# Kernel tuning notes

Hardware: AMD Instinct MI355X
Metric: run time of the kernel (lower is better)

The kernel has to match this reference:

```python
import jax, jax.numpy as jnp
import numpy as np

H = 1024  # hidden_size
B, N = 64, 512
NEG = 1e30


def setup_inputs() -> dict:
    key = jax.random.key(0)
    ks = jax.random.split(key, 10)
    Q = jax.random.normal(ks[0], (B, H), dtype=jnp.float32)
    K = jax.random.normal(ks[1], (B, N, H), dtype=jnp.float32)
    V = jax.random.normal(ks[2], (B, N, H), dtype=jnp.float32)
    adj = jax.random.randint(ks[3], (B, N), 0, 2, dtype=jnp.int32)
    s_mask = jax.random.randint(ks[4], (B, N), 0, 2, dtype=jnp.int32)
    o_mask = jax.random.randint(ks[5], (B, N), 0, 2, dtype=jnp.int32)
    # learned params (torch nn.Linear conventions: y = x @ W.T + b)
    lim = 1.0 / np.sqrt(2 * H)
    W_att = jax.random.uniform(ks[6], (1, 2 * H), minval=-lim, maxval=lim, dtype=jnp.float32)
    b_att = jax.random.uniform(ks[7], (1,), minval=-lim, maxval=lim, dtype=jnp.float32)
    limh = 1.0 / np.sqrt(H)
    Wr0 = jax.random.uniform(ks[8], (H, H), minval=-limh, maxval=limh, dtype=jnp.float32)
    Wr1 = jax.random.uniform(ks[9], (H, H), minval=-limh, maxval=limh, dtype=jnp.float32)
    return {"Q": Q, "K": K, "V": V, "adj": adj, "s_mask": s_mask, "o_mask": o_mask,
            "W_att": W_att, "b_att": b_att, "Wr0": Wr0, "Wr1": Wr1}


def reference(Q, K, V, adj, s_mask, o_mask, W_att, b_att, Wr0, Wr1):
    # concat-score: Linear([Q;K]) == Q @ Wq.T + K @ Wk.T + b (avoids materializing [B,N,2H])
    Wq, Wk = W_att[:, :H], W_att[:, H:]  # each [1, H]
    q_score = Q @ Wq.T                    # [B, 1]
    k_score = jnp.einsum('bnh,oh->bn', K, Wk)  # [B, N]
    alpha = (q_score + k_score + b_att)[:, None, :]  # [B, 1, N]
    # adjacency mask
    adj_f = adj.astype(jnp.float32)[:, None, :]      # [B, 1, N]
    alpha = alpha - (1.0 - adj_f) * NEG
    attn_weight = jax.nn.softmax(alpha, axis=2)      # [B, 1, N]
    # dual value projections gated by speaker/other masks
    V0 = jnp.einsum('bnh,oh->bno', V, Wr0)           # [B, N, H]
    V1 = jnp.einsum('bnh,oh->bno', V, Wr1)
    s = s_mask.astype(jnp.float32)[:, :, None]
    o = o_mask.astype(jnp.float32)[:, :, None]
    Vg = V0 * s + V1 * o                             # [B, N, H]
    attn_sum = jnp.einsum('bon,bnh->boh', attn_weight, Vg)[:, 0]  # [B, H]
    return (attn_weight, attn_sum)
```

## Files before the change

### kernel.cpp

```cpp
#include <hip/hip_runtime.h>
#include <math.h>

#define HDIM 1024
#define INVB (1 << 13)
#define SBIT (1 << 14)
#define OBIT (1 << 15)
#define SLOTS 10
#define CH 32

__global__ __launch_bounds__(256) void k_fusedA(const float* __restrict__ Kmat,
                                                const float* __restrict__ V,
                                                const int* __restrict__ adj,
                                                const int* __restrict__ sm,
                                                const int* __restrict__ om,
                                                const float* __restrict__ Wk,
                                                float* __restrict__ e_out,
                                                float* __restrict__ p0,
                                                float* __restrict__ p1) {
    __shared__ int segc[8];
    __shared__ int codeL[CH];
    __shared__ float2 eso[CH];
    __shared__ float2 cw[CH + 8];
    __shared__ int cn[CH + 8];
    __shared__ int s_cnz8;
    int b = blockIdx.x / SLOTS;
    int chunk = blockIdx.x - b * SLOTS;
    int tid = threadIdx.x, wave = tid >> 6, lane = tid & 63;
    int gb = b * 512;
    int start = chunk * CH;
    size_t pbase = ((size_t)(chunk * 64 + b)) * HDIM + tid * 4;

    int r0w = wave * 128;
    int a0p = adj[gb + r0w + lane] != 0;
    int a1p = adj[gb + r0w + 64 + lane] != 0;
    unsigned long long m0 = __ballot(a0p);
    unsigned long long m1 = __ballot(a1p);
    if (lane == 0) {
        segc[wave * 2]     = __popcll(m0);
        segc[wave * 2 + 1] = __popcll(m1);
    }
    __syncthreads();
    int tot = 0;
#pragma unroll
    for (int i = 0; i < 8; ++i) tot += segc[i];
    int kp = (tot + CH - 1) & ~(CH - 1);
    if (start >= kp) {
        float4 z = {0.f, 0.f, 0.f, 0.f};
        *(float4*)(p0 + pbase) = z;
        *(float4*)(p1 + pbase) = z;
        return;
    }
    {
        unsigned long long lt = (1ull << lane) - 1ull;
        int base = 0;
#pragma unroll
        for (int i = 0; i < 8; ++i) if (i < wave * 2) base += segc[i];
        int pos0 = base + __popcll(m0 & lt);
        if (a0p && pos0 >= start && pos0 < start + CH) {
            int r = r0w + lane;
            codeL[pos0 - start] = r | (sm[gb + r] ? SBIT : 0) | (om[gb + r] ? OBIT : 0);
        }
        int base1 = base + __popcll(m0);
        int pos1 = base1 + __popcll(m1 & lt);
        if (a1p && pos1 >= start && pos1 < start + CH) {
            int r = r0w + 64 + lane;
            codeL[pos1 - start] = r | (sm[gb + r] ? SBIT : 0) | (om[gb + r] ? OBIT : 0);
        }
    }
    if (tid < CH && start + tid >= tot) codeL[tid] = INVB;
    const float4* wk4 = (const float4*)Wk;
    float4 wk0 = wk4[lane], wk1 = wk4[64 + lane],
           wk2 = wk4[128 + lane], wk3 = wk4[192 + lane];
    __syncthreads();

#pragma unroll
    for (int pp = 0; pp < 4; ++pp) {
        int rr = wave * 8 + pp * 2;
        int c0 = codeL[rr], c1 = codeL[rr + 1];
        int n0 = c0 & 511, n1 = c1 & 511;
        const float4* kq0 = (const float4*)(Kmat + (size_t)(gb + n0) * HDIM);
        const float4* kq1 = (const float4*)(Kmat + (size_t)(gb + n1) * HDIM);
        float4 a0 = kq0[lane],       a1 = kq0[64 + lane],
               a2 = kq0[128 + lane], a3 = kq0[192 + lane];
        float4 d0 = kq1[lane],       d1 = kq1[64 + lane],
               d2 = kq1[128 + lane], d3 = kq1[192 + lane];
        __builtin_amdgcn_sched_barrier(0);

        float s0 = 0.f, s1 = 0.f;
        s0 = fmaf(a0.x, wk0.x, s0); s0 = fmaf(a0.y, wk0.y, s0);
        s0 = fmaf(a0.z, wk0.z, s0); s0 = fmaf(a0.w, wk0.w, s0);
        s0 = fmaf(a1.x, wk1.x, s0); s0 = fmaf(a1.y, wk1.y, s0);
        s0 = fmaf(a1.z, wk1.z, s0); s0 = fmaf(a1.w, wk1.w, s0);
        s0 = fmaf(a2.x, wk2.x, s0); s0 = fmaf(a2.y, wk2.y, s0);
        s0 = fmaf(a2.z, wk2.z, s0); s0 = fmaf(a2.w, wk2.w, s0);
        s0 = fmaf(a3.x, wk3.x, s0); s0 = fmaf(a3.y, wk3.y, s0);
        s0 = fmaf(a3.z, wk3.z, s0); s0 = fmaf(a3.w, wk3.w, s0);
        s1 = fmaf(d0.x, wk0.x, s1); s1 = fmaf(d0.y, wk0.y, s1);
        s1 = fmaf(d0.z, wk0.z, s1); s1 = fmaf(d0.w, wk0.w, s1);
        s1 = fmaf(d1.x, wk1.x, s1); s1 = fmaf(d1.y, wk1.y, s1);
        s1 = fmaf(d1.z, wk1.z, s1); s1 = fmaf(d1.w, wk1.w, s1);
        s1 = fmaf(d2.x, wk2.x, s1); s1 = fmaf(d2.y, wk2.y, s1);
        s1 = fmaf(d2.z, wk2.z, s1); s1 = fmaf(d2.w, wk2.w, s1);
        s1 = fmaf(d3.x, wk3.x, s1); s1 = fmaf(d3.y, wk3.y, s1);
        s1 = fmaf(d3.z, wk3.z, s1); s1 = fmaf(d3.w, wk3.w, s1);

#pragma unroll
        for (int off = 32; off; off >>= 1) {
            s0 += __shfl_xor(s0, off);
            s1 += __shfl_xor(s1, off);
        }
        if (lane == 0) {
            float e0 = expf(s0), e1 = expf(s1);
            if (!(c0 & INVB)) e_out[gb + n0] = e0;
            if (!(c1 & INVB)) e_out[gb + n1] = e1;
            eso[rr]     = make_float2((c0 & SBIT) ? e0 : 0.f, (c0 & OBIT) ? e0 : 0.f);
            eso[rr + 1] = make_float2((c1 & SBIT) ? e1 : 0.f, (c1 & OBIT) ? e1 : 0.f);
        }
    }
    __syncthreads();

    if (wave == 0) {
        bool pred = (lane < CH) && ((codeL[lane] & (SBIT | OBIT)) != 0) &&
                    !(codeL[lane] & INVB);
        unsigned long long m = __ballot(pred);
        int cnz = __popcll(m);
        if (pred) {
            int pos = __popcll(m & ((1ull << lane) - 1ull));
            cn[pos] = codeL[lane] & 511;
            cw[pos] = eso[lane];
        }
        int cnz8 = (cnz + 7) & ~7;
        if (lane >= CH && lane < CH + 8) {
            int p = cnz + (lane - CH);
            if (p < cnz8) { cn[p] = 0; cw[p] = make_float2(0.f, 0.f); }
        }
        if (lane == 0) s_cnz8 = cnz8;
    }
    __syncthreads();

    int cnz8 = s_cnz8;
    const float* Vb = V + (size_t)gb * HDIM;
    float4 a0 = {0.f, 0.f, 0.f, 0.f};
    float4 a1 = {0.f, 0.f, 0.f, 0.f};
    for (int g = 0; g < cnz8; g += 8) {
        int nn[8]; float2 ww[8];
#pragma unroll
        for (int i = 0; i < 8; ++i) { nn[i] = cn[g + i]; ww[i] = cw[g + i]; }
        float4 v[8];
#pragma unroll
        for (int i = 0; i < 8; ++i)
            v[i] = *((const float4*)(Vb + (size_t)nn[i] * HDIM) + tid);
        __builtin_amdgcn_sched_barrier(0);
#pragma unroll
        for (int i = 0; i < 8; ++i) {
            a0.x = fmaf(ww[i].x, v[i].x, a0.x); a0.y = fmaf(ww[i].x, v[i].y, a0.y);
            a0.z = fmaf(ww[i].x, v[i].z, a0.z); a0.w = fmaf(ww[i].x, v[i].w, a0.w);
            a1.x = fmaf(ww[i].y, v[i].x, a1.x); a1.y = fmaf(ww[i].y, v[i].y, a1.y);
            a1.z = fmaf(ww[i].y, v[i].z, a1.z); a1.w = fmaf(ww[i].y, v[i].w, a1.w);
        }
    }
    *(float4*)(p0 + pbase) = a0;
    *(float4*)(p1 + pbase) = a1;
}

__global__ __launch_bounds__(512) void k_denomredu(const float* __restrict__ e,
                                                   const int* __restrict__ adj,
                                                   const float* __restrict__ p0,
                                                   const float* __restrict__ p1,
                                                   float* __restrict__ w_out,
                                                   float* __restrict__ u0,
                                                   float* __restrict__ u1) {
    __shared__ float red[8];
    int b = blockIdx.x;
    int tid = threadIdx.x;
    int wave = tid >> 6, lane = tid & 63;
    int idx = b * 512 + tid;

    float ev = adj[idx] ? e[idx] : 0.f;
    float t = ev;
#pragma unroll
    for (int off = 32; off; off >>= 1) t += __shfl_xor(t, off);
    if (lane == 0) red[wave] = t;
    __syncthreads();
    float tot = red[0];
#pragma unroll
    for (int i = 1; i < 8; ++i) tot += red[i];
    float inv = 1.f / tot;
    w_out[idx] = ev * inv;

    const float* p = (tid < 256) ? p0 : p1;
    float* u = (tid < 256) ? u0 : u1;
    int h4 = tid & 255;
    float4 a = {0.f, 0.f, 0.f, 0.f};
#pragma unroll
    for (int s = 0; s < SLOTS; ++s) {
        float4 v = *(const float4*)(p + ((size_t)(s * 64 + b)) * HDIM + h4 * 4);
        a.x += v.x; a.y += v.y; a.z += v.z; a.w += v.w;
    }
    a.x *= inv; a.y *= inv; a.z *= inv; a.w *= inv;
    *(float4*)(u + (size_t)b * HDIM + h4 * 4) = a;
}

__global__ __launch_bounds__(256) void k_out(const float* __restrict__ u0,
                                             const float* __restrict__ u1,
                                             const float* __restrict__ Wr0,
                                             const float* __restrict__ Wr1,
                                             float* __restrict__ pOut) {
    __shared__ float lds[64 * 128];
    int tid = threadIdx.x;
    int ht = blockIdx.x >> 4;
    int kc = blockIdx.x & 15;
    const float* usrc = (kc < 8) ? u0 : u1;
    const float* wsrc = (kc < 8) ? Wr0 : Wr1;
    int koff = (kc & 7) * 128;
    int h0 = ht * 64;

    {
        int c4 = tid & 31;
        int r2 = tid >> 5;
#pragma unroll
        for (int i = 0; i < 8; ++i) {
            int row = i * 8 + r2;
            float4 v = *(const float4*)(usrc + (size_t)row * HDIM + koff + c4 * 4);
            *(float4*)&lds[row * 128 + ((c4 ^ (row & 7)) << 2)] = v;
        }
    }
    __syncthreads();

    int b = tid & 63;
    int wu = __builtin_amdgcn_readfirstlane(tid >> 6);
    int hbase = h0 + wu * 16;
    const float* wrow = wsrc + (size_t)hbase * HDIM + koff;

    float acc[16];
#pragma unroll
    for (int j = 0; j < 16; ++j) acc[j] = 0.f;

#pragma unroll 4
    for (int k4 = 0; k4 < 32; ++k4) {
        float4 uv = *(float4*)&lds[b * 128 + ((k4 ^ (b & 7)) << 2)];
#pragma unroll
        for (int j = 0; j < 16; ++j) {
            float4 wv = *(const float4*)(wrow + (size_t)j * HDIM + k4 * 4);
            acc[j] = fmaf(uv.x, wv.x, acc[j]);
            acc[j] = fmaf(uv.y, wv.y, acc[j]);
            acc[j] = fmaf(uv.z, wv.z, acc[j]);
            acc[j] = fmaf(uv.w, wv.w, acc[j]);
        }
    }
#pragma unroll
    for (int j = 0; j < 16; ++j)
        pOut[((size_t)kc * HDIM + hbase + j) * 64 + b] = acc[j];
}

__global__ __launch_bounds__(256) void k_redout(const float* __restrict__ pOut,
                                                float* __restrict__ out1) {
    int tid = threadIdx.x;
    int b = tid & 63;
    int h = blockIdx.x * 4 + (tid >> 6);
    float acc = 0.f;
#pragma unroll
    for (int kc = 0; kc < 16; ++kc)
        acc += pOut[((size_t)kc * HDIM + h) * 64 + b];
    out1[(size_t)b * HDIM + h] = acc;
}

extern "C" void kernel_launch(void* const* d_in, const int* in_sizes, int n_in,
                              void* d_out, int out_size, void* d_ws, size_t ws_size,
                              hipStream_t stream) {
    const float* Kmat  = (const float*)d_in[1];
    const float* V     = (const float*)d_in[2];
    const int*   adj   = (const int*)d_in[3];
    const int*   smask = (const int*)d_in[4];
    const int*   omask = (const int*)d_in[5];
    const float* Watt  = (const float*)d_in[6];
    const float* Wr0   = (const float*)d_in[8];
    const float* Wr1   = (const float*)d_in[9];
    float* out = (float*)d_out;
    float* ws  = (float*)d_ws;

    float* e    = ws;
    float* p0   = ws + 32768;
    float* p1   = ws + 688128;
    float* u0   = ws + 1343488;
    float* u1   = ws + 1409024;
    float* pOut = ws + 1474560;
    const float* Wk = Watt + HDIM;

    k_fusedA   <<<64 * SLOTS, 256, 0, stream>>>(Kmat, V, adj, smask, omask, Wk, e, p0, p1);
    k_denomredu<<<        64, 512, 0, stream>>>(e, adj, p0, p1, out, u0, u1);
    k_out      <<<       256, 256, 0, stream>>>(u0, u1, Wr0, Wr1, pOut);
    k_redout   <<<       256, 256, 0, stream>>>(pOut, out + 32768);
}
```

Before: 63.45 us.

## Split score and weighted-V passes; partition V gather by hidden octant

The fused score+V-gather kernel is split into three kernels: one computes exp scores for adjacent rows, one computes the softmax denominator and weights, and a new weighted-V kernel compacts the active rows per batch. Each block of that kernel handles one 128-column slice of H and reduces partial sums in LDS. This removes the large per-chunk partial buffers (p0/p1) and their cross-slot reduction pass, and V blocks no longer depend on the chunk split of the score pass. In exchange it adds a kernel launch and rereads e, adj and the masks from global memory.

Measured after the change: 64.13 us. No clear change (+1.1%).

```diff
diff --git a/kernel.cpp b/kernel.cpp
--- a/kernel.cpp
+++ b/kernel.cpp
@@ -3,32 +3,20 @@
 
 #define HDIM 1024
 #define INVB (1 << 13)
-#define SBIT (1 << 14)
-#define OBIT (1 << 15)
-#define SLOTS 10
-#define CH 32
-
-__global__ __launch_bounds__(256) void k_fusedA(const float* __restrict__ Kmat,
-                                                const float* __restrict__ V,
-                                                const int* __restrict__ adj,
-                                                const int* __restrict__ sm,
-                                                const int* __restrict__ om,
-                                                const float* __restrict__ Wk,
-                                                float* __restrict__ e_out,
-                                                float* __restrict__ p0,
-                                                float* __restrict__ p1) {
+#define SCH 32
+#define SSLOTS 10
+
+__global__ __launch_bounds__(256) void k_scoresE(const float* __restrict__ Kmat,
+                                                 const int* __restrict__ adj,
+                                                 const float* __restrict__ Wk,
+                                                 float* __restrict__ e_out) {
     __shared__ int segc[8];
-    __shared__ int codeL[CH];
-    __shared__ float2 eso[CH];
-    __shared__ float2 cw[CH + 8];
-    __shared__ int cn[CH + 8];
-    __shared__ int s_cnz8;
-    int b = blockIdx.x / SLOTS;
-    int chunk = blockIdx.x - b * SLOTS;
+    __shared__ int codeL[SCH];
+    int b = blockIdx.x / SSLOTS;
+    int chunk = blockIdx.x - b * SSLOTS;
     int tid = threadIdx.x, wave = tid >> 6, lane = tid & 63;
     int gb = b * 512;
-    int start = chunk * CH;
-    size_t pbase = ((size_t)(chunk * 64 + b)) * HDIM + tid * 4;
+    int start = chunk * SCH;
 
     int r0w = wave * 128;
     int a0p = adj[gb + r0w + lane] != 0;
@@ -43,31 +31,21 @@
     int tot = 0;
 #pragma unroll
     for (int i = 0; i < 8; ++i) tot += segc[i];
-    int kp = (tot + CH - 1) & ~(CH - 1);
-    if (start >= kp) {
-        float4 z = {0.f, 0.f, 0.f, 0.f};
-        *(float4*)(p0 + pbase) = z;
-        *(float4*)(p1 + pbase) = z;
-        return;
-    }
+    if (start >= tot) return;
     {
         unsigned long long lt = (1ull << lane) - 1ull;
         int base = 0;
 #pragma unroll
         for (int i = 0; i < 8; ++i) if (i < wave * 2) base += segc[i];
         int pos0 = base + __popcll(m0 & lt);
-        if (a0p && pos0 >= start && pos0 < start + CH) {
-            int r = r0w + lane;
-            codeL[pos0 - start] = r | (sm[gb + r] ? SBIT : 0) | (om[gb + r] ? OBIT : 0);
-        }
+        if (a0p && pos0 >= start && pos0 < start + SCH)
+            codeL[pos0 - start] = r0w + lane;
         int base1 = base + __popcll(m0);
         int pos1 = base1 + __popcll(m1 & lt);
-        if (a1p && pos1 >= start && pos1 < start + CH) {
-            int r = r0w + 64 + lane;
-            codeL[pos1 - start] = r | (sm[gb + r] ? SBIT : 0) | (om[gb + r] ? OBIT : 0);
-        }
-    }
-    if (tid < CH && start + tid >= tot) codeL[tid] = INVB;
+        if (a1p && pos1 >= start && pos1 < start + SCH)
+            codeL[pos1 - start] = r0w + 64 + lane;
+    }
+    if (tid < SCH && start + tid >= tot) codeL[tid] = INVB;
     const float4* wk4 = (const float4*)Wk;
     float4 wk0 = wk4[lane], wk1 = wk4[64 + lane],
            wk2 = wk4[128 + lane], wk3 = wk4[192 + lane];
@@ -110,46 +88,115 @@
             s1 += __shfl_xor(s1, off);
         }
         if (lane == 0) {
-            float e0 = expf(s0), e1 = expf(s1);
-            if (!(c0 & INVB)) e_out[gb + n0] = e0;
-            if (!(c1 & INVB)) e_out[gb + n1] = e1;
-            eso[rr]     = make_float2((c0 & SBIT) ? e0 : 0.f, (c0 & OBIT) ? e0 : 0.f);
-            eso[rr + 1] = make_float2((c1 & SBIT) ? e1 : 0.f, (c1 & OBIT) ? e1 : 0.f);
-        }
-    }
-    __syncthreads();
-
-    if (wave == 0) {
-        bool pred = (lane < CH) && ((codeL[lane] & (SBIT | OBIT)) != 0) &&
-                    !(codeL[lane] & INVB);
-        unsigned long long m = __ballot(pred);
-        int cnz = __popcll(m);
-        if (pred) {
-            int pos = __popcll(m & ((1ull << lane) - 1ull));
-            cn[pos] = codeL[lane] & 511;
-            cw[pos] = eso[lane];
-        }
-        int cnz8 = (cnz + 7) & ~7;
-        if (lane >= CH && lane < CH + 8) {
-            int p = cnz + (lane - CH);
-            if (p < cnz8) { cn[p] = 0; cw[p] = make_float2(0.f, 0.f); }
-        }
-        if (lane == 0) s_cnz8 = cnz8;
-    }
-    __syncthreads();
-
-    int cnz8 = s_cnz8;
-    const float* Vb = V + (size_t)gb * HDIM;
+            if (!(c0 & INVB)) e_out[gb + n0] = expf(s0);
+            if (!(c1 & INVB)) e_out[gb + n1] = expf(s1);
+        }
+    }
+}
+
+__global__ __launch_bounds__(512) void k_denom(const float* __restrict__ e,
+                                               const int* __restrict__ adj,
+                                               float* __restrict__ w_out,
+                                               float* __restrict__ invArr) {
+    __shared__ float red[8];
+    int b = blockIdx.x;
+    int tid = threadIdx.x;
+    int wave = tid >> 6, lane = tid & 63;
+    int idx = b * 512 + tid;
+
+    float ev = adj[idx] ? e[idx] : 0.f;
+    float t = ev;
+#pragma unroll
+    for (int off = 32; off; off >>= 1) t += __shfl_xor(t, off);
+    if (lane == 0) red[wave] = t;
+    __syncthreads();
+    float tot = red[0];
+#pragma unroll
+    for (int i = 1; i < 8; ++i) tot += red[i];
+    float inv = 1.f / tot;
+    w_out[idx] = ev * inv;
+    if (tid == 0) invArr[b] = inv;
+}
+
+__global__ __launch_bounds__(256) void k_weightv(const float* __restrict__ V,
+                                                 const int* __restrict__ adj,
+                                                 const int* __restrict__ sm,
+                                                 const int* __restrict__ om,
+                                                 const float* __restrict__ e,
+                                                 const float* __restrict__ invArr,
+                                                 float* __restrict__ u0,
+                                                 float* __restrict__ u1) {
+    __shared__ int segc[8];
+    __shared__ int cn[512];
+    __shared__ float2 cw[512];
+    __shared__ float4 comb[448];
+    int b = blockIdx.x >> 3;
+    int oct = blockIdx.x & 7;
+    int tid = threadIdx.x, wave = tid >> 6, lane = tid & 63;
+    int gb = b * 512;
+
+    int r0w = wave * 128;
+    int ra = gb + r0w + lane;
+    int rb = ra + 64;
+    int sa = sm[ra], oa = om[ra];
+    int sb = sm[rb], ob = om[rb];
+    int pa = (adj[ra] != 0) && ((sa | oa) != 0);
+    int pb = (adj[rb] != 0) && ((sb | ob) != 0);
+    unsigned long long m0 = __ballot(pa);
+    unsigned long long m1 = __ballot(pb);
+    if (lane == 0) {
+        segc[wave * 2]     = __popcll(m0);
+        segc[wave * 2 + 1] = __popcll(m1);
+    }
+    __syncthreads();
+    int tot = 0;
+#pragma unroll
+    for (int i = 0; i < 8; ++i) tot += segc[i];
+    {
+        unsigned long long lt = (1ull << lane) - 1ull;
+        int base = 0;
+#pragma unroll
+        for (int i = 0; i < 8; ++i) if (i < wave * 2) base += segc[i];
+        if (pa) {
+            int pos = base + __popcll(m0 & lt);
+            float ev = e[ra];
+            cn[pos] = r0w + lane;
+            cw[pos] = make_float2(sa ? ev : 0.f, oa ? ev : 0.f);
+        }
+        int base1 = base + __popcll(m0);
+        if (pb) {
+            int pos = base1 + __popcll(m1 & lt);
+            float ev = e[rb];
+            cn[pos] = r0w + 64 + lane;
+            cw[pos] = make_float2(sb ? ev : 0.f, ob ? ev : 0.f);
+        }
+    }
+    __syncthreads();
+    int cnt64 = (tot + 63) & ~63;
+    if (cnt64 > 512) cnt64 = 512;
+    if (tid < 64 && tot + tid < cnt64) {
+        cn[tot + tid] = 0;
+        cw[tot + tid] = make_float2(0.f, 0.f);
+    }
+    __syncthreads();
+
+    int slot = tid & 31;
+    int rsub = tid >> 5;
+    const float4* Vb4 = (const float4*)(V + (size_t)gb * HDIM) + oct * 32 + slot;
     float4 a0 = {0.f, 0.f, 0.f, 0.f};
     float4 a1 = {0.f, 0.f, 0.f, 0.f};
-    for (int g = 0; g < cnz8; g += 8) {
+    for (int base = 0; base < cnt64; base += 64) {
         int nn[8]; float2 ww[8];
 #pragma unroll
-        for (int i = 0; i < 8; ++i) { nn[i] = cn[g + i]; ww[i] = cw[g + i]; }
+        for (int i = 0; i < 8; ++i) {
+            int idx = base + i * 8 + rsub;
+            nn[i] = cn[idx];
+            ww[i] = cw[idx];
+        }
         float4 v[8];
 #pragma unroll
         for (int i = 0; i < 8; ++i)
-            v[i] = *((const float4*)(Vb + (size_t)nn[i] * HDIM) + tid);
+            v[i] = Vb4[(size_t)nn[i] * 256];
         __builtin_amdgcn_sched_barrier(0);
 #pragma unroll
         for (int i = 0; i < 8; ++i) {
@@ -159,46 +206,27 @@
             a1.z = fmaf(ww[i].y, v[i].z, a1.z); a1.w = fmaf(ww[i].y, v[i].w, a1.w);
         }
     }
-    *(float4*)(p0 + pbase) = a0;
-    *(float4*)(p1 + pbase) = a1;
-}
-
-__global__ __launch_bounds__(512) void k_denomredu(const float* __restrict__ e,
-                                                   const int* __restrict__ adj,
-                                                   const float* __restrict__ p0,
-                                                   const float* __restrict__ p1,
-                                                   float* __restrict__ w_out,
-                                                   float* __restrict__ u0,
-                                                   float* __restrict__ u1) {
-    __shared__ float red[8];
-    int b = blockIdx.x;
-    int tid = threadIdx.x;
-    int wave = tid >> 6, lane = tid & 63;
-    int idx = b * 512 + tid;
-
-    float ev = adj[idx] ? e[idx] : 0.f;
-    float t = ev;
-#pragma unroll
-    for (int off = 32; off; off >>= 1) t += __shfl_xor(t, off);
-    if (lane == 0) red[wave] = t;
-    __syncthreads();
-    float tot = red[0];
-#pragma unroll
-    for (int i = 1; i < 8; ++i) tot += red[i];
-    float inv = 1.f / tot;
-    w_out[idx] = ev * inv;
-
-    const float* p = (tid < 256) ? p0 : p1;
-    float* u = (tid < 256) ? u0 : u1;
-    int h4 = tid & 255;
-    float4 a = {0.f, 0.f, 0.f, 0.f};
-#pragma unroll
-    for (int s = 0; s < SLOTS; ++s) {
-        float4 v = *(const float4*)(p + ((size_t)(s * 64 + b)) * HDIM + h4 * 4);
-        a.x += v.x; a.y += v.y; a.z += v.z; a.w += v.w;
-    }
-    a.x *= inv; a.y *= inv; a.z *= inv; a.w *= inv;
-    *(float4*)(u + (size_t)b * HDIM + h4 * 4) = a;
+
+    if (rsub > 0) {
+        comb[(rsub - 1) * 32 + slot] = a0;
+        comb[224 + (rsub - 1) * 32 + slot] = a1;
+    }
+    __syncthreads();
+    if (rsub == 0) {
+#pragma unroll
+        for (int i = 0; i < 7; ++i) {
+            float4 c0 = comb[i * 32 + slot];
+            float4 c1 = comb[224 + i * 32 + slot];
+            a0.x += c0.x; a0.y += c0.y; a0.z += c0.z; a0.w += c0.w;
+            a1.x += c1.x; a1.y += c1.y; a1.z += c1.z; a1.w += c1.w;
+        }
+        float iv = invArr[b];
+        a0.x *= iv; a0.y *= iv; a0.z *= iv; a0.w *= iv;
+        a1.x *= iv; a1.y *= iv; a1.z *= iv; a1.w *= iv;
+        size_t o = (size_t)b * HDIM + oct * 128 + slot * 4;
+        *(float4*)(u0 + o) = a0;
+        *(float4*)(u1 + o) = a1;
+    }
 }
 
 __global__ __launch_bounds__(256) void k_out(const float* __restrict__ u0,
@@ -280,15 +308,15 @@
     float* ws  = (float*)d_ws;
 
     float* e    = ws;
-    float* p0   = ws + 32768;
-    float* p1   = ws + 688128;
-    float* u0   = ws + 1343488;
-    float* u1   = ws + 1409024;
-    float* pOut = ws + 1474560;
+    float* inv  = ws + 32768;
+    float* u0   = ws + 32896;
+    float* u1   = ws + 98432;
+    float* pOut = ws + 163968;
     const float* Wk = Watt + HDIM;
 
-    k_fusedA   <<<64 * SLOTS, 256, 0, stream>>>(Kmat, V, adj, smask, omask, Wk, e, p0, p1);
-    k_denomredu<<<        64, 512, 0, stream>>>(e, adj, p0, p1, out, u0, u1);
-    k_out      <<<       256, 256, 0, stream>>>(u0, u1, Wr0, Wr1, pOut);
-    k_redout   <<<       256, 256, 0, stream>>>(pOut, out + 32768);
-}
+    k_scoresE<<<64 * SSLOTS, 256, 0, stream>>>(Kmat, adj, Wk, e);
+    k_denom  <<<        64, 512, 0, stream>>>(e, adj, out, inv);
+    k_weightv<<<       512, 256, 0, stream>>>(V, adj, smask, omask, e, inv, u0, u1);
+    k_out    <<<       256, 256, 0, stream>>>(u0, u1, Wr0, Wr1, pOut);
+    k_redout <<<       256, 256, 0, stream>>>(pOut, out + 32768);
+}
```
